# Optimization experiments

Measured on AMD Instinct MI355X. Metric: run time of the kernel, lower is better.

## Reference

```python
import jax, jax.numpy as jnp
import numpy as np

B, N, K = 8, 2048, 16          # clouds, points per cloud, knn k
C_IN, C_OUT, H = 64, 128, 64   # channels; H = hidden of pos_nn/attn_nn MLPs


def _init(key, shape, fan_in):
    return jax.random.normal(key, shape, jnp.float32) / np.sqrt(fan_in)


def setup_inputs() -> dict:
    key = jax.random.key(0)
    ks = jax.random.split(key, 20)
    P = B * N
    inp = {
        "x": jax.random.normal(ks[0], (P, C_IN), jnp.float32),
        "pos": jax.random.uniform(ks[1], (P, 3), jnp.float32),
        "batch": jnp.arange(P, dtype=jnp.int64 if jax.config.jax_enable_x64 else jnp.int32) // N,
        # lin_in: in->in, bias
        "Wi": _init(ks[2], (C_IN, C_IN), C_IN), "bi": jnp.zeros((C_IN,), jnp.float32),
        # PointTransformerConv: lin_src/lin_dst/lin are bias-free Linear(in, out)
        "Wsrc": _init(ks[3], (C_IN, C_OUT), C_IN),
        "Wdst": _init(ks[4], (C_IN, C_OUT), C_IN),
        "Wlin": _init(ks[5], (C_IN, C_OUT), C_IN),
        # pos_nn = MLP([3, 64, out], norm=None, plain_last=False): Lin-ReLU-Lin-ReLU
        "Wp1": _init(ks[6], (3, H), 3), "bp1": jnp.zeros((H,), jnp.float32),
        "Wp2": _init(ks[7], (H, C_OUT), H), "bp2": jnp.zeros((C_OUT,), jnp.float32),
        # attn_nn = MLP([out, 64, out], norm=None, plain_last=False)
        "Wa1": _init(ks[8], (C_OUT, H), C_OUT), "ba1": jnp.zeros((H,), jnp.float32),
        "Wa2": _init(ks[9], (H, C_OUT), H), "ba2": jnp.zeros((C_OUT,), jnp.float32),
        # lin_out: out->out, bias
        "Wo": _init(ks[10], (C_OUT, C_OUT), C_OUT), "bo": jnp.zeros((C_OUT,), jnp.float32),
    }
    return inp


def _knn_with_self(pn):
    # pn: [B,N,3] -> neighbor indices [B,N,K+1] = {self} U kNN (excl self),
    # matching knn_graph(loop=False) followed by conv's add_self_loops.
    sq = jnp.sum(pn * pn, -1)                                   # [B,N]
    d2 = sq[:, :, None] + sq[:, None, :] - 2.0 * jnp.einsum("bnd,bmd->bnm", pn, pn)
    d2 = d2 + jnp.eye(N, dtype=pn.dtype) * 1e10                 # exclude self
    _, idx = jax.lax.top_k(-d2, K)                              # [B,N,K]
    self_idx = jnp.broadcast_to(jnp.arange(N)[None, :, None], (B, N, 1))
    return jnp.concatenate([self_idx, idx], axis=-1)            # [B,N,K+1]


def _forward(x, pos, batch, Wi, bi, Wsrc, Wdst, Wlin, Wp1, bp1, Wp2, bp2,
             Wa1, ba1, Wa2, ba2, Wo, bo):
    # batch is structured as B equal-size clouds of N points (see setup_inputs);
    # knn is computed per-cloud, equivalent to knn_graph(pos, k, batch).
    h = jax.nn.relu(x @ Wi + bi).reshape(B, N, C_IN)            # lin_in + relu
    pn = pos.reshape(B, N, 3)
    nbr = _knn_with_self(pn)                                    # [B,N,K+1]

    gather = jax.vmap(lambda t, i: t[i])                        # [N,C],[N,K+1]->[N,K+1,C]

    a_src = h @ Wsrc                                            # [B,N,C_OUT]
    a_dst = h @ Wdst
    v = h @ Wlin

    rel = pn[:, :, None, :] - gather(pn, nbr)                   # pos_i - pos_j [B,N,K+1,3]
    delta = jax.nn.relu(jax.nn.relu(rel @ Wp1 + bp1) @ Wp2 + bp2)   # pos_nn

    alpha = a_dst[:, :, None, :] - gather(a_src, nbr) + delta   # alpha_i - alpha_j + delta
    attn = jax.nn.relu(jax.nn.relu(alpha @ Wa1 + ba1) @ Wa2 + ba2)  # attn_nn
    w = jax.nn.softmax(attn, axis=2)                            # softmax over neighbors

    msg = w * (gather(v, nbr) + delta)                          # [B,N,K+1,C_OUT]
    out = jnp.mean(msg, axis=2)                                 # aggr='mean' (PyG default here)
    out = out.reshape(B * N, C_OUT)
    return jax.nn.relu(out @ Wo + bo)                           # lin_out + relu


def reference(x, pos, batch, Wi, bi, Wsrc, Wdst, Wlin, Wp1, bp1, Wp2, bp2,
              Wa1, ba1, Wa2, ba2, Wo, bo):
    return _forward(x, pos, batch, Wi, bi, Wsrc, Wdst, Wlin, Wp1, bp1, Wp2, bp2,
                    Wa1, ba1, Wa2, ba2, Wo, bo)
```

## Files before the change

kernel.cpp:

```cpp
#include <hip/hip_runtime.h>
#include <hip/hip_fp16.h>

typedef _Float16 h8 __attribute__((ext_vector_type(8)));
typedef _Float16 h4 __attribute__((ext_vector_type(4)));
typedef float fx4 __attribute__((ext_vector_type(4)));

#define NPTS   2048
#define KP1    17
#define PGPT   4
#define EDGES  68
#define ROWS   80
#define MT     5
#define DELTA_OFF 0
#define PH_OFF    20480
#define ATT_OFF   30720
#define SJ_OFF    30720
#define NBR_OFF   52224
#define EDGE_SMEM 52544
#define ATT_RB    168

__device__ __forceinline__ int swzA(int row, int bytecol) {
  return (row << 7) + (bytecol ^ ((row & 7) << 4));
}
__device__ __forceinline__ int swzB(int row, int bytecol) {
  return (row << 8) + (bytecol ^ ((row & 7) << 4));
}

#define GH_NB    256
#define WP_NB    32
#define P1_GRID  (GH_NB + WP_NB)

__global__ __launch_bounds__(512) void phase1_kernel(
    const float* __restrict__ x, const float* __restrict__ Wi, const float* __restrict__ bi,
    float* __restrict__ h,
    const float* __restrict__ Wdst, const float* __restrict__ Wsrc,
    const float* __restrict__ Wlin, const float* __restrict__ Wa1,
    float* __restrict__ Wall)
{
  __shared__ __align__(16) char buf[33792];
  const int bid = blockIdx.x;
  const int tid = threadIdx.x;

  if (bid < GH_NB) {
    float* As = (float*)buf;
    float* Ws = (float*)(buf + 64 * 68 * 4);
    long row0 = (long)bid * 64;
    {
      int r = tid >> 3, k8 = (tid & 7) * 8;
      float4 a0 = *(const float4*)(x + (row0 + r) * 64 + k8);
      float4 a1 = *(const float4*)(x + (row0 + r) * 64 + k8 + 4);
      *(float4*)&As[r * 68 + k8] = a0;
      *(float4*)&As[r * 68 + k8 + 4] = a1;
      float4 w0 = *(const float4*)(Wi + r * 64 + k8);
      float4 w1 = *(const float4*)(Wi + r * 64 + k8 + 4);
      *(float4*)&Ws[r * 64 + k8] = w0;
      *(float4*)&Ws[r * 64 + k8 + 4] = w1;
    }
    __syncthreads();
    int tx = tid & 15, ty = tid >> 4;
    float acc[2][4] = {};
#pragma unroll 8
    for (int k = 0; k < 64; ++k) {
      float4 w = *(const float4*)&Ws[k * 64 + tx * 4];
      float a0 = As[(ty * 2 + 0) * 68 + k];
      float a1 = As[(ty * 2 + 1) * 68 + k];
      acc[0][0] += a0 * w.x; acc[0][1] += a0 * w.y; acc[0][2] += a0 * w.z; acc[0][3] += a0 * w.w;
      acc[1][0] += a1 * w.x; acc[1][1] += a1 * w.y; acc[1][2] += a1 * w.z; acc[1][3] += a1 * w.w;
    }
    float b0 = bi[tx * 4 + 0], b1 = bi[tx * 4 + 1], b2 = bi[tx * 4 + 2], b3 = bi[tx * 4 + 3];
#pragma unroll
    for (int i = 0; i < 2; ++i) {
      float4 o;
      o.x = fmaxf(acc[i][0] + b0, 0.f); o.y = fmaxf(acc[i][1] + b1, 0.f);
      o.z = fmaxf(acc[i][2] + b2, 0.f); o.w = fmaxf(acc[i][3] + b3, 0.f);
      *(float4*)(h + (row0 + ty * 2 + i) * 64 + tx * 4) = o;
    }
  } else {
    int gid = (bid - GH_NB) * 512 + tid;
    int q = gid >> 12, r = (gid >> 6) & 63, c = gid & 63;
    float val;
    if (q < 2) {
      const float* W = q ? Wsrc : Wdst;
      float acc = 0.f;
      for (int k = 0; k < 128; ++k) acc += W[r * 128 + k] * Wa1[k * 64 + c];
      val = acc;
    } else {
      val = Wlin[r * 128 + (q - 2) * 64 + c];
    }
    Wall[r * 256 + q * 64 + c] = val;
  }
}

#define KNN_NB 2048
#define UG_NB  1024
#define PK_NB  80
#define K2_GRID (KNN_NB + UG_NB + PK_NB)

__global__ __launch_bounds__(512) void knn_usv_kernel(
    const float* __restrict__ pos, int* __restrict__ nbr, float* __restrict__ rel,
    const float* __restrict__ h, const float* __restrict__ Wall,
    float* __restrict__ usv,
    const float* __restrict__ Wp2, const float* __restrict__ Wa1,
    const float* __restrict__ Wa2, const float* __restrict__ Wo,
    _Float16* __restrict__ p2p, _Float16* __restrict__ a1p, _Float16* __restrict__ a2p,
    _Float16* __restrict__ wop)
{
  __shared__ __align__(16) char buf[33792];
  const int bid = blockIdx.x;
  const int tid = threadIdx.x;

  if (bid < KNN_NB) {
    float* px  = (float*)buf;
    float* py  = (float*)(buf + 8192);
    float* pz  = (float*)(buf + 16384);
    float* sqs = (float*)(buf + 24576);
    int p0 = bid * 8;
    int base = (p0 >> 11) << 11;
    for (int i = tid; i < NPTS; i += 512) {
      float xx = pos[(size_t)(base + i) * 3 + 0];
      float yy = pos[(size_t)(base + i) * 3 + 1];
      float zz = pos[(size_t)(base + i) * 3 + 2];
      px[i] = xx; py[i] = yy; pz[i] = zz;
      sqs[i] = xx * xx + yy * yy + zz * zz;
    }
    __syncthreads();
    int wid = tid >> 6, lane = tid & 63;
    int pl = (p0 & 2047) + wid;
    int gp = base + pl;
    float pix = px[pl], piy = py[pl], piz = pz[pl];

    unsigned key[8];
#pragma unroll
    for (int i = 0; i < 8; ++i) key[i] = 0xFFFFFFFFu;
#pragma unroll
    for (int t = 0; t < 32; ++t) {
      int j = t * 64 + lane;
      float dot = pix * px[j] + piy * py[j] + piz * pz[j];
      float dp = __builtin_fmaf(-2.f, dot, sqs[j]) + 4.0f;
      unsigned kb = (__float_as_uint(dp) & 0xFFFFFFE0u) | (unsigned)t;
      kb = (j == pl) ? 0xFFFFFFFFu : kb;
#pragma unroll
      for (int i = 0; i < 8; ++i) {
        unsigned lo = min(key[i], kb), hi = max(key[i], kb);
        key[i] = lo; kb = hi;
      }
    }

    double pxd = (double)pix, pyd = (double)piy, pzd = (double)piz;
    double sqi64 = pxd * pxd + pyd * pyd + pzd * pzd;
    unsigned long long kk[8];
#pragma unroll
    for (int i = 0; i < 8; ++i) {
      if (key[i] == 0xFFFFFFFFu) { kk[i] = 0xFFFFFFFFFFFFFFFFull; continue; }
      int t = key[i] & 31;
      int j = t * 64 + lane;
      double xj = (double)px[j], yj = (double)py[j], zj = (double)pz[j];
      double sqj = xj * xj + yj * yj + zj * zj;
      double dot = pxd * xj + pyd * yj + pzd * zj;
      double d2 = sqi64 + sqj - 2.0 * dot;
      d2 = d2 > 0.0 ? d2 : 0.0;
      unsigned long long bits = (unsigned long long)__double_as_longlong(d2);
      kk[i] = (bits & ~0x7FFull) | (unsigned long long)j;
    }
#define CE(a, b) { unsigned long long lo_ = kk[a] < kk[b] ? kk[a] : kk[b]; \
                   unsigned long long hi_ = kk[a] < kk[b] ? kk[b] : kk[a]; \
                   kk[a] = lo_; kk[b] = hi_; }
    CE(0,1) CE(2,3) CE(4,5) CE(6,7)
    CE(0,2) CE(1,3) CE(4,6) CE(5,7)
    CE(1,2) CE(5,6) CE(0,4) CE(3,7)
    CE(1,5) CE(2,6)
    CE(1,4) CE(3,6)
    CE(2,4) CE(3,5)
    CE(3,4)
#undef CE

    if (lane == 0) nbr[gp * KP1] = gp;
    if (lane < 3)  rel[(size_t)gp * KP1 * 3 + lane] = 0.f;
    for (int it = 0; it < 16; ++it) {
      unsigned h32 = (unsigned)(kk[0] >> 32);
      unsigned key2 = (h32 & ~63u) | (unsigned)lane;
      unsigned m2 = key2;
#pragma unroll
      for (int off = 32; off > 0; off >>= 1) {
        unsigned o = __shfl_xor(m2, off);
        m2 = o < m2 ? o : m2;
      }
      bool same = ((key2 ^ m2) >> 6) == 0;
      unsigned long long ball = __ballot(same);
      int wl; unsigned jwin;
      if (__popcll(ball) == 1) {
        wl = (int)(m2 & 63u);
        unsigned lo32 = (unsigned)kk[0];
        unsigned wlo = __shfl(lo32, wl);
        jwin = wlo & 2047u;
      } else {
        unsigned long long mk = same ? kk[0] : 0xFFFFFFFFFFFFFFFFull;
#pragma unroll
        for (int off = 32; off > 0; off >>= 1) {
          unsigned long long o = __shfl_xor(mk, off);
          mk = o < mk ? o : mk;
        }
        jwin = (unsigned)(mk & 2047ull);
        wl = (int)(jwin & 63u);
      }
      if (lane == 0) nbr[gp * KP1 + 1 + it] = base + (int)jwin;
      if (lane < 3) {
        const float* ps = lane == 0 ? px : (lane == 1 ? py : pz);
        float pi = lane == 0 ? pix : (lane == 1 ? piy : piz);
        rel[((size_t)gp * KP1 + 1 + it) * 3 + lane] = pi - ps[(int)jwin];
      }
      bool mine = (lane == wl);
#pragma unroll
      for (int i = 0; i < 7; ++i) kk[i] = mine ? kk[i + 1] : kk[i];
      kk[7] = mine ? 0xFFFFFFFFFFFFFFFFull : kk[7];
    }
  } else if (bid < KNN_NB + UG_NB) {
    float* As = (float*)buf;
    float* Ws = (float*)(buf + 64 * 68 * 4);
    int b2 = bid - KNN_NB;
    long row0 = (long)(b2 >> 2) * 64;
    int c0 = (b2 & 3) * 64;
    {
      int r = tid >> 3, k8 = (tid & 7) * 8;
      float4 a0 = *(const float4*)(h + (row0 + r) * 64 + k8);
      float4 a1 = *(const float4*)(h + (row0 + r) * 64 + k8 + 4);
      *(float4*)&As[r * 68 + k8] = a0;
      *(float4*)&As[r * 68 + k8 + 4] = a1;
      float4 w0 = *(const float4*)(Wall + r * 256 + c0 + k8);
      float4 w1 = *(const float4*)(Wall + r * 256 + c0 + k8 + 4);
      *(float4*)&Ws[r * 64 + k8] = w0;
      *(float4*)&Ws[r * 64 + k8 + 4] = w1;
    }
    __syncthreads();
    int tx = tid & 15, ty = tid >> 4;
    float acc[2][4] = {};
#pragma unroll 8
    for (int k = 0; k < 64; ++k) {
      float4 w = *(const float4*)&Ws[k * 64 + tx * 4];
      float a0 = As[(ty * 2 + 0) * 68 + k];
      float a1 = As[(ty * 2 + 1) * 68 + k];
      acc[0][0] += a0 * w.x; acc[0][1] += a0 * w.y; acc[0][2] += a0 * w.z; acc[0][3] += a0 * w.w;
      acc[1][0] += a1 * w.x; acc[1][1] += a1 * w.y; acc[1][2] += a1 * w.z; acc[1][3] += a1 * w.w;
    }
#pragma unroll
    for (int i = 0; i < 2; ++i) {
      float4 o;
      o.x = acc[i][0]; o.y = acc[i][1]; o.z = acc[i][2]; o.w = acc[i][3];
      *(float4*)(usv + (row0 + ty * 2 + i) * 256 + c0 + tx * 4) = o;
    }
  } else {
    int gid = (bid - KNN_NB - UG_NB) * 512 + tid;
    if (gid < 24576) {
      int m = gid >> 13;
      int r = gid & 8191;
      int tl = r >> 9;
      int l  = (r >> 3) & 63;
      int j  = r & 7;
      const float* src; _Float16* dst; int N, kt, nt;
      if (m == 0)      { src = Wp2; dst = p2p; N = 128; kt = tl & 1; nt = tl >> 1; }
      else if (m == 1) { src = Wa1; dst = a1p; N = 64;  kt = tl & 3; nt = tl >> 2; }
      else             { src = Wa2; dst = a2p; N = 128; kt = tl & 1; nt = tl >> 1; }
      int k = kt * 32 + (l >> 4) * 8 + j;
      int n = nt * 16 + (l & 15);
      dst[r] = (_Float16)src[k * N + n];
    } else {
      int r = gid - 24576;
      int tl = r >> 9;
      int l  = (r >> 3) & 63;
      int j  = r & 7;
      int kt = tl & 3, nt = tl >> 2;
      int k = kt * 32 + (l >> 4) * 8 + j;
      int n = nt * 16 + (l & 15);
      wop[r] = (_Float16)Wo[k * 128 + n];
    }
  }
}

__global__ __launch_bounds__(512, 6) void edge_kernel(
    const int* __restrict__ nbr,
    const float* __restrict__ usv,
    const float* __restrict__ rel,
    const float* __restrict__ Wp1, const float* __restrict__ bp1,
    const float* __restrict__ bp2, const float* __restrict__ ba1, const float* __restrict__ ba2,
    const _Float16* __restrict__ Wp2p, const _Float16* __restrict__ Wa1p, const _Float16* __restrict__ Wa2p,
    const _Float16* __restrict__ Wop, const float* __restrict__ bo,
    float* __restrict__ out)
{
  __shared__ __align__(16) char smem[EDGE_SMEM];
  int* nbr_s = (int*)(smem + NBR_OFF);
  const int tid = threadIdx.x;
  const int lane = tid & 63;
  const int wid = tid >> 6;
  const int bid = blockIdx.x;
  const int pb = ((bid & 7) << 9) | (bid >> 3);
  const int p0 = pb * PGPT;

  const int pp5 = tid >> 7;
  const int c5 = tid & 127;
  float vreg[KP1];
  {
    const int* __restrict__ nrow = nbr + (size_t)(p0 + pp5) * KP1;
#pragma unroll
    for (int k = 0; k < KP1; ++k) {
      int jv = nrow[k];
      vreg[k] = usv[(size_t)jv * 256 + 128 + c5];
    }
  }

  if (tid < ROWS) nbr_s[tid] = (tid < EDGES) ? nbr[p0 * KP1 + tid] : p0;
  __syncthreads();

  {
    float w1x = Wp1[lane], w1y = Wp1[64 + lane], w1z = Wp1[128 + lane], b1 = bp1[lane];
    float b1a = ba1[lane];
    const float* relb = rel + (size_t)p0 * (KP1 * 3);
    for (int e = wid; e < ROWS; e += 8) {
      int eb = __builtin_amdgcn_readfirstlane(min(e, EDGES - 1));
      int p  = (eb * 241) >> 12;
      int j  = __builtin_amdgcn_readfirstlane(nbr_s[eb]);
      float sv = usv[(size_t)j * 256 + 64 + lane];
      float uu = usv[(size_t)(p0 + p) * 256 + lane];
      *(_Float16*)(smem + SJ_OFF + swzA(e, lane * 2)) = (_Float16)(uu - sv + b1a);
      float rx = relb[eb * 3 + 0];
      float ry = relb[eb * 3 + 1];
      float rz = relb[eb * 3 + 2];
      float acc = fmaxf(b1 + rx * w1x + ry * w1y + rz * w1z, 0.f);
      *(_Float16*)(smem + PH_OFF + swzA(e, lane * 2)) = (_Float16)acc;
    }
  }
  __syncthreads();

  const int rl = lane & 15;
  const int kl = lane >> 4;

  {
    int nt = wid;
    h8 b0 = *(const h8*)(Wp2p + ((size_t)(nt * 2 + 0) * 64 + lane) * 8);
    h8 b1 = *(const h8*)(Wp2p + ((size_t)(nt * 2 + 1) * 64 + lane) * 8);
    int col = nt * 16 + rl;
    float bias2 = bp2[col];
    for (int mt = 0; mt < MT; ++mt) {
      int arow = mt * 16 + rl;
      h8 a0 = *(const h8*)(smem + PH_OFF + swzA(arow, kl * 16));
      h8 a1 = *(const h8*)(smem + PH_OFF + swzA(arow, 64 + kl * 16));
      fx4 acc = {0.f, 0.f, 0.f, 0.f};
      acc = __builtin_amdgcn_mfma_f32_16x16x32_f16(a0, b0, acc, 0, 0, 0);
      acc = __builtin_amdgcn_mfma_f32_16x16x32_f16(a1, b1, acc, 0, 0, 0);
#pragma unroll
      for (int jj = 0; jj < 4; ++jj) {
        int orow = mt * 16 + kl * 4 + jj;
        float val = fmaxf(acc[jj] + bias2, 0.f);
        *(_Float16*)(smem + DELTA_OFF + swzB(orow, col * 2)) = (_Float16)val;
      }
    }
  }
  __syncthreads();

  {
    int nt = wid & 3;
    h8 b[4];
#pragma unroll
    for (int kt = 0; kt < 4; ++kt)
      b[kt] = *(const h8*)(Wa1p + ((size_t)(nt * 4 + kt) * 64 + lane) * 8);
    int hcol = nt * 16 + rl;
    for (int mt = (wid >> 2); mt < MT; mt += 2) {
      int arow = mt * 16 + rl;
      fx4 acc = {0.f, 0.f, 0.f, 0.f};
#pragma unroll
      for (int kt = 0; kt < 4; ++kt) {
        h8 a = *(const h8*)(smem + DELTA_OFF + swzB(arow, kt * 64 + kl * 16));
        acc = __builtin_amdgcn_mfma_f32_16x16x32_f16(a, b[kt], acc, 0, 0, 0);
      }
#pragma unroll
      for (int jj = 0; jj < 4; ++jj) {
        int orow = mt * 16 + kl * 4 + jj;
        float bb = (float)*(const _Float16*)(smem + SJ_OFF + swzA(orow, hcol * 2));
        float val = fmaxf(acc[jj] + bb, 0.f);
        *(_Float16*)(smem + PH_OFF + swzA(orow, hcol * 2)) = (_Float16)val;
      }
    }
  }
  __syncthreads();

  {
    int nt = wid;
    h8 b0 = *(const h8*)(Wa2p + ((size_t)(nt * 2 + 0) * 64 + lane) * 8);
    h8 b1 = *(const h8*)(Wa2p + ((size_t)(nt * 2 + 1) * 64 + lane) * 8);
    int col = nt * 16 + rl;
    float b2v = ba2[col];
    char* cbase = smem + ATT_OFF + col * ATT_RB;
    for (int mt = 0; mt < MT; ++mt) {
      int arow = mt * 16 + rl;
      h8 a0 = *(const h8*)(smem + PH_OFF + swzA(arow, kl * 16));
      h8 a1 = *(const h8*)(smem + PH_OFF + swzA(arow, 64 + kl * 16));
      fx4 acc = {0.f, 0.f, 0.f, 0.f};
      acc = __builtin_amdgcn_mfma_f32_16x16x32_f16(a0, b0, acc, 0, 0, 0);
      acc = __builtin_amdgcn_mfma_f32_16x16x32_f16(a1, b1, acc, 0, 0, 0);
#pragma unroll
      for (int jj = 0; jj < 4; ++jj) {
        int orow = mt * 16 + kl * 4 + jj;
        if (orow < EDGES) {
          int pp = (orow * 241) >> 12;
          float val = fmaxf(acc[jj] + b2v, 0.f);
          *(_Float16*)(cbase + (orow + 3 * pp) * 2) = (_Float16)val;
        }
      }
    }
  }
  __syncthreads();

  h8 bw[4];
#pragma unroll
  for (int kt = 0; kt < 4; ++kt)
    bw[kt] = *(const h8*)(Wop + ((size_t)(wid * 4 + kt) * 64 + lane) * 8);

  {
    int r0 = pp5 * KP1;
    const char* abase = smem + ATT_OFF + c5 * ATT_RB + pp5 * 40;
    h4 t0 = *(const h4*)(abase + 0);
    h4 t1 = *(const h4*)(abase + 8);
    h4 t2 = *(const h4*)(abase + 16);
    h4 t3 = *(const h4*)(abase + 24);
    float att[KP1];
#pragma unroll
    for (int q = 0; q < 4; ++q) {
      att[0 + q]  = (float)t0[q];
      att[4 + q]  = (float)t1[q];
      att[8 + q]  = (float)t2[q];
      att[12 + q] = (float)t3[q];
    }
    att[16] = (float)*(const _Float16*)(abase + 32);
    float m8[8];
#pragma unroll
    for (int k = 0; k < 8; ++k) m8[k] = fmaxf(att[k], att[k + 8]);
    float m4a = fmaxf(m8[0], m8[1]), m4b = fmaxf(m8[2], m8[3]);
    float m4c = fmaxf(m8[4], m8[5]), m4d = fmaxf(m8[6], m8[7]);
    float m = fmaxf(fmaxf(fmaxf(m4a, m4b), fmaxf(m4c, m4d)), att[16]);
    float den = 0.f;
#pragma unroll
    for (int k = 0; k < KP1; ++k) { att[k] = __expf(att[k] - m); den += att[k]; }
    float inv = 1.f / (den * 17.f);
    float acc = 0.f;
#pragma unroll
    for (int k = 0; k < KP1; ++k) {
      float dd = (float)*(const _Float16*)(smem + DELTA_OFF + swzB(r0 + k, c5 * 2));
      acc += att[k] * (vreg[k] + dd);
    }
    *(_Float16*)(smem + PH_OFF + swzB(pp5, c5 * 2)) = (_Float16)(acc * inv);
  }
  __syncthreads();

  {
    fx4 acc = {0.f, 0.f, 0.f, 0.f};
#pragma unroll
    for (int kt = 0; kt < 4; ++kt) {
      h8 a = *(const h8*)(smem + PH_OFF + swzB(rl, kt * 64 + kl * 16));
      acc = __builtin_amdgcn_mfma_f32_16x16x32_f16(a, bw[kt], acc, 0, 0, 0);
    }
    if (kl == 0) {
      int col = wid * 16 + rl;
      float bov = bo[col];
#pragma unroll
      for (int jj = 0; jj < 4; ++jj)
        out[(size_t)(p0 + jj) * 128 + col] = fmaxf(acc[jj] + bov, 0.f);
    }
  }
}

extern "C" void kernel_launch(void* const* d_in, const int* in_sizes, int n_in,
                              void* d_out, int out_size, void* d_ws, size_t ws_size,
                              hipStream_t stream) {
  const float* x    = (const float*)d_in[0];
  const float* pos  = (const float*)d_in[1];
  const float* Wi   = (const float*)d_in[3];
  const float* bi   = (const float*)d_in[4];
  const float* Wsrc = (const float*)d_in[5];
  const float* Wdst = (const float*)d_in[6];
  const float* Wlin = (const float*)d_in[7];
  const float* Wp1  = (const float*)d_in[8];
  const float* bp1  = (const float*)d_in[9];
  const float* Wp2  = (const float*)d_in[10];
  const float* bp2  = (const float*)d_in[11];
  const float* Wa1  = (const float*)d_in[12];
  const float* ba1  = (const float*)d_in[13];
  const float* Wa2  = (const float*)d_in[14];
  const float* ba2  = (const float*)d_in[15];
  const float* Wo   = (const float*)d_in[16];
  const float* bo   = (const float*)d_in[17];
  float* out = (float*)d_out;

  char* ws = (char*)d_ws;
  float* h    = (float*)(ws + 0);
  float* usv  = (float*)(ws + 4194304);
  float* Wall = (float*)(ws + 20971520);
  float* rel  = (float*)(ws + 21037056);
  int*   nbr  = (int*)  (ws + 29360128);
  _Float16* p2p = (_Float16*)(ws + 30474240);
  _Float16* a1p = (_Float16*)(ws + 30490624);
  _Float16* a2p = (_Float16*)(ws + 30507008);
  _Float16* wop = (_Float16*)(ws + 30523392);

  phase1_kernel<<<P1_GRID, 512, 0, stream>>>(x, Wi, bi, h, Wdst, Wsrc, Wlin, Wa1, Wall);
  knn_usv_kernel<<<K2_GRID, 512, 0, stream>>>(pos, nbr, rel, h, Wall, usv,
                                              Wp2, Wa1, Wa2, Wo, p2p, a1p, a2p, wop);
  edge_kernel<<<4096, 512, 0, stream>>>(nbr, usv, rel, Wp1, bp1, bp2, ba1, ba2,
                                        p2p, a1p, a2p, wop, bo, out);
}
```

Measured before the change: 136.9 us.

## Co-schedule kNN with h and weight prep, split usv GEMM into own kernel

```diff
diff --git a/kernel.cpp b/kernel.cpp
--- a/kernel.cpp
+++ b/kernel.cpp
@@ -26,82 +26,21 @@
   return (row << 8) + (bytecol ^ ((row & 7) << 4));
 }
 
-#define GH_NB    256
-#define WP_NB    32
-#define P1_GRID  (GH_NB + WP_NB)
-
-__global__ __launch_bounds__(512) void phase1_kernel(
+#define KNN_NB 2048
+#define GH_NB  256
+#define WP_NB  32
+#define PK_NB  80
+#define A_GRID (KNN_NB + GH_NB + WP_NB + PK_NB)
+
+__global__ __launch_bounds__(512) void frontA_kernel(
+    const float* __restrict__ pos, int* __restrict__ nbr, float* __restrict__ rel,
     const float* __restrict__ x, const float* __restrict__ Wi, const float* __restrict__ bi,
     float* __restrict__ h,
     const float* __restrict__ Wdst, const float* __restrict__ Wsrc,
     const float* __restrict__ Wlin, const float* __restrict__ Wa1,
-    float* __restrict__ Wall)
-{
-  __shared__ __align__(16) char buf[33792];
-  const int bid = blockIdx.x;
-  const int tid = threadIdx.x;
-
-  if (bid < GH_NB) {
-    float* As = (float*)buf;
-    float* Ws = (float*)(buf + 64 * 68 * 4);
-    long row0 = (long)bid * 64;
-    {
-      int r = tid >> 3, k8 = (tid & 7) * 8;
-      float4 a0 = *(const float4*)(x + (row0 + r) * 64 + k8);
-      float4 a1 = *(const float4*)(x + (row0 + r) * 64 + k8 + 4);
-      *(float4*)&As[r * 68 + k8] = a0;
-      *(float4*)&As[r * 68 + k8 + 4] = a1;
-      float4 w0 = *(const float4*)(Wi + r * 64 + k8);
-      float4 w1 = *(const float4*)(Wi + r * 64 + k8 + 4);
-      *(float4*)&Ws[r * 64 + k8] = w0;
-      *(float4*)&Ws[r * 64 + k8 + 4] = w1;
-    }
-    __syncthreads();
-    int tx = tid & 15, ty = tid >> 4;
-    float acc[2][4] = {};
-#pragma unroll 8
-    for (int k = 0; k < 64; ++k) {
-      float4 w = *(const float4*)&Ws[k * 64 + tx * 4];
-      float a0 = As[(ty * 2 + 0) * 68 + k];
-      float a1 = As[(ty * 2 + 1) * 68 + k];
-      acc[0][0] += a0 * w.x; acc[0][1] += a0 * w.y; acc[0][2] += a0 * w.z; acc[0][3] += a0 * w.w;
-      acc[1][0] += a1 * w.x; acc[1][1] += a1 * w.y; acc[1][2] += a1 * w.z; acc[1][3] += a1 * w.w;
-    }
-    float b0 = bi[tx * 4 + 0], b1 = bi[tx * 4 + 1], b2 = bi[tx * 4 + 2], b3 = bi[tx * 4 + 3];
-#pragma unroll
-    for (int i = 0; i < 2; ++i) {
-      float4 o;
-      o.x = fmaxf(acc[i][0] + b0, 0.f); o.y = fmaxf(acc[i][1] + b1, 0.f);
-      o.z = fmaxf(acc[i][2] + b2, 0.f); o.w = fmaxf(acc[i][3] + b3, 0.f);
-      *(float4*)(h + (row0 + ty * 2 + i) * 64 + tx * 4) = o;
-    }
-  } else {
-    int gid = (bid - GH_NB) * 512 + tid;
-    int q = gid >> 12, r = (gid >> 6) & 63, c = gid & 63;
-    float val;
-    if (q < 2) {
-      const float* W = q ? Wsrc : Wdst;
-      float acc = 0.f;
-      for (int k = 0; k < 128; ++k) acc += W[r * 128 + k] * Wa1[k * 64 + c];
-      val = acc;
-    } else {
-      val = Wlin[r * 128 + (q - 2) * 64 + c];
-    }
-    Wall[r * 256 + q * 64 + c] = val;
-  }
-}
-
-#define KNN_NB 2048
-#define UG_NB  1024
-#define PK_NB  80
-#define K2_GRID (KNN_NB + UG_NB + PK_NB)
-
-__global__ __launch_bounds__(512) void knn_usv_kernel(
-    const float* __restrict__ pos, int* __restrict__ nbr, float* __restrict__ rel,
-    const float* __restrict__ h, const float* __restrict__ Wall,
-    float* __restrict__ usv,
-    const float* __restrict__ Wp2, const float* __restrict__ Wa1,
-    const float* __restrict__ Wa2, const float* __restrict__ Wo,
+    float* __restrict__ Wall,
+    const float* __restrict__ Wp2, const float* __restrict__ Wa2,
+    const float* __restrict__ Wo,
     _Float16* __restrict__ p2p, _Float16* __restrict__ a1p, _Float16* __restrict__ a2p,
     _Float16* __restrict__ wop)
 {
@@ -110,24 +49,22 @@
   const int tid = threadIdx.x;
 
   if (bid < KNN_NB) {
-    float* px  = (float*)buf;
-    float* py  = (float*)(buf + 8192);
-    float* pz  = (float*)(buf + 16384);
-    float* sqs = (float*)(buf + 24576);
+    float4* pc = (float4*)buf;
     int p0 = bid * 8;
     int base = (p0 >> 11) << 11;
     for (int i = tid; i < NPTS; i += 512) {
       float xx = pos[(size_t)(base + i) * 3 + 0];
       float yy = pos[(size_t)(base + i) * 3 + 1];
       float zz = pos[(size_t)(base + i) * 3 + 2];
-      px[i] = xx; py[i] = yy; pz[i] = zz;
-      sqs[i] = xx * xx + yy * yy + zz * zz;
+      float4 v; v.x = xx; v.y = yy; v.z = zz; v.w = xx * xx + yy * yy + zz * zz;
+      pc[i] = v;
     }
     __syncthreads();
     int wid = tid >> 6, lane = tid & 63;
     int pl = (p0 & 2047) + wid;
     int gp = base + pl;
-    float pix = px[pl], piy = py[pl], piz = pz[pl];
+    float4 qp = pc[pl];
+    float pix = qp.x, piy = qp.y, piz = qp.z;
 
     unsigned key[8];
 #pragma unroll
@@ -135,8 +72,9 @@
 #pragma unroll
     for (int t = 0; t < 32; ++t) {
       int j = t * 64 + lane;
-      float dot = pix * px[j] + piy * py[j] + piz * pz[j];
-      float dp = __builtin_fmaf(-2.f, dot, sqs[j]) + 4.0f;
+      float4 c = pc[j];
+      float dot = pix * c.x + piy * c.y + piz * c.z;
+      float dp = __builtin_fmaf(-2.f, dot, c.w) + 4.0f;
       unsigned kb = (__float_as_uint(dp) & 0xFFFFFFE0u) | (unsigned)t;
       kb = (j == pl) ? 0xFFFFFFFFu : kb;
 #pragma unroll
@@ -154,7 +92,8 @@
       if (key[i] == 0xFFFFFFFFu) { kk[i] = 0xFFFFFFFFFFFFFFFFull; continue; }
       int t = key[i] & 31;
       int j = t * 64 + lane;
-      double xj = (double)px[j], yj = (double)py[j], zj = (double)pz[j];
+      float4 c = pc[j];
+      double xj = (double)c.x, yj = (double)c.y, zj = (double)c.z;
       double sqj = xj * xj + yj * yj + zj * zj;
       double dot = pxd * xj + pyd * yj + pzd * zj;
       double d2 = sqi64 + sqj - 2.0 * dot;
@@ -205,29 +144,27 @@
       }
       if (lane == 0) nbr[gp * KP1 + 1 + it] = base + (int)jwin;
       if (lane < 3) {
-        const float* ps = lane == 0 ? px : (lane == 1 ? py : pz);
         float pi = lane == 0 ? pix : (lane == 1 ? piy : piz);
-        rel[((size_t)gp * KP1 + 1 + it) * 3 + lane] = pi - ps[(int)jwin];
+        float pj = ((const float*)&pc[(int)jwin])[lane];
+        rel[((size_t)gp * KP1 + 1 + it) * 3 + lane] = pi - pj;
       }
       bool mine = (lane == wl);
 #pragma unroll
       for (int i = 0; i < 7; ++i) kk[i] = mine ? kk[i + 1] : kk[i];
       kk[7] = mine ? 0xFFFFFFFFFFFFFFFFull : kk[7];
     }
-  } else if (bid < KNN_NB + UG_NB) {
+  } else if (bid < KNN_NB + GH_NB) {
     float* As = (float*)buf;
     float* Ws = (float*)(buf + 64 * 68 * 4);
-    int b2 = bid - KNN_NB;
-    long row0 = (long)(b2 >> 2) * 64;
-    int c0 = (b2 & 3) * 64;
+    long row0 = (long)(bid - KNN_NB) * 64;
     {
       int r = tid >> 3, k8 = (tid & 7) * 8;
-      float4 a0 = *(const float4*)(h + (row0 + r) * 64 + k8);
-      float4 a1 = *(const float4*)(h + (row0 + r) * 64 + k8 + 4);
+      float4 a0 = *(const float4*)(x + (row0 + r) * 64 + k8);
+      float4 a1 = *(const float4*)(x + (row0 + r) * 64 + k8 + 4);
       *(float4*)&As[r * 68 + k8] = a0;
       *(float4*)&As[r * 68 + k8 + 4] = a1;
-      float4 w0 = *(const float4*)(Wall + r * 256 + c0 + k8);
-      float4 w1 = *(const float4*)(Wall + r * 256 + c0 + k8 + 4);
+      float4 w0 = *(const float4*)(Wi + r * 64 + k8);
+      float4 w1 = *(const float4*)(Wi + r * 64 + k8 + 4);
       *(float4*)&Ws[r * 64 + k8] = w0;
       *(float4*)&Ws[r * 64 + k8 + 4] = w1;
     }
@@ -242,14 +179,29 @@
       acc[0][0] += a0 * w.x; acc[0][1] += a0 * w.y; acc[0][2] += a0 * w.z; acc[0][3] += a0 * w.w;
       acc[1][0] += a1 * w.x; acc[1][1] += a1 * w.y; acc[1][2] += a1 * w.z; acc[1][3] += a1 * w.w;
     }
+    float b0 = bi[tx * 4 + 0], b1 = bi[tx * 4 + 1], b2 = bi[tx * 4 + 2], b3 = bi[tx * 4 + 3];
 #pragma unroll
     for (int i = 0; i < 2; ++i) {
       float4 o;
-      o.x = acc[i][0]; o.y = acc[i][1]; o.z = acc[i][2]; o.w = acc[i][3];
-      *(float4*)(usv + (row0 + ty * 2 + i) * 256 + c0 + tx * 4) = o;
-    }
+      o.x = fmaxf(acc[i][0] + b0, 0.f); o.y = fmaxf(acc[i][1] + b1, 0.f);
+      o.z = fmaxf(acc[i][2] + b2, 0.f); o.w = fmaxf(acc[i][3] + b3, 0.f);
+      *(float4*)(h + (row0 + ty * 2 + i) * 64 + tx * 4) = o;
+    }
+  } else if (bid < KNN_NB + GH_NB + WP_NB) {
+    int gid = (bid - KNN_NB - GH_NB) * 512 + tid;
+    int q = gid >> 12, r = (gid >> 6) & 63, c = gid & 63;
+    float val;
+    if (q < 2) {
+      const float* W = q ? Wsrc : Wdst;
+      float acc = 0.f;
+      for (int k = 0; k < 128; ++k) acc += W[r * 128 + k] * Wa1[k * 64 + c];
+      val = acc;
+    } else {
+      val = Wlin[r * 128 + (q - 2) * 64 + c];
+    }
+    Wall[r * 256 + q * 64 + c] = val;
   } else {
-    int gid = (bid - KNN_NB - UG_NB) * 512 + tid;
+    int gid = (bid - KNN_NB - GH_NB - WP_NB) * 512 + tid;
     if (gid < 24576) {
       int m = gid >> 13;
       int r = gid & 8191;
@@ -276,6 +228,47 @@
   }
 }
 
+__global__ __launch_bounds__(512) void usv_kernel(
+    const float* __restrict__ h, const float* __restrict__ Wall,
+    float* __restrict__ usv)
+{
+  __shared__ __align__(16) char buf[33792];
+  const int tid = threadIdx.x;
+  float* As = (float*)buf;
+  float* Ws = (float*)(buf + 64 * 68 * 4);
+  int b2 = blockIdx.x;
+  long row0 = (long)(b2 >> 2) * 64;
+  int c0 = (b2 & 3) * 64;
+  {
+    int r = tid >> 3, k8 = (tid & 7) * 8;
+    float4 a0 = *(const float4*)(h + (row0 + r) * 64 + k8);
+    float4 a1 = *(const float4*)(h + (row0 + r) * 64 + k8 + 4);
+    *(float4*)&As[r * 68 + k8] = a0;
+    *(float4*)&As[r * 68 + k8 + 4] = a1;
+    float4 w0 = *(const float4*)(Wall + r * 256 + c0 + k8);
+    float4 w1 = *(const float4*)(Wall + r * 256 + c0 + k8 + 4);
+    *(float4*)&Ws[r * 64 + k8] = w0;
+    *(float4*)&Ws[r * 64 + k8 + 4] = w1;
+  }
+  __syncthreads();
+  int tx = tid & 15, ty = tid >> 4;
+  float acc[2][4] = {};
+#pragma unroll 8
+  for (int k = 0; k < 64; ++k) {
+    float4 w = *(const float4*)&Ws[k * 64 + tx * 4];
+    float a0 = As[(ty * 2 + 0) * 68 + k];
+    float a1 = As[(ty * 2 + 1) * 68 + k];
+    acc[0][0] += a0 * w.x; acc[0][1] += a0 * w.y; acc[0][2] += a0 * w.z; acc[0][3] += a0 * w.w;
+    acc[1][0] += a1 * w.x; acc[1][1] += a1 * w.y; acc[1][2] += a1 * w.z; acc[1][3] += a1 * w.w;
+  }
+#pragma unroll
+  for (int i = 0; i < 2; ++i) {
+    float4 o;
+    o.x = acc[i][0]; o.y = acc[i][1]; o.z = acc[i][2]; o.w = acc[i][3];
+    *(float4*)(usv + (row0 + ty * 2 + i) * 256 + c0 + tx * 4) = o;
+  }
+}
+
 __global__ __launch_bounds__(512, 6) void edge_kernel(
     const int* __restrict__ nbr,
     const float* __restrict__ usv,
@@ -500,9 +493,10 @@
   _Float16* a2p = (_Float16*)(ws + 30507008);
   _Float16* wop = (_Float16*)(ws + 30523392);
 
-  phase1_kernel<<<P1_GRID, 512, 0, stream>>>(x, Wi, bi, h, Wdst, Wsrc, Wlin, Wa1, Wall);
-  knn_usv_kernel<<<K2_GRID, 512, 0, stream>>>(pos, nbr, rel, h, Wall, usv,
-                                              Wp2, Wa1, Wa2, Wo, p2p, a1p, a2p, wop);
+  frontA_kernel<<<A_GRID, 512, 0, stream>>>(pos, nbr, rel, x, Wi, bi, h,
+                                            Wdst, Wsrc, Wlin, Wa1, Wall,
+                                            Wp2, Wa2, Wo, p2p, a1p, a2p, wop);
+  usv_kernel<<<1024, 512, 0, stream>>>(h, Wall, usv);
   edge_kernel<<<4096, 512, 0, stream>>>(nbr, usv, rel, Wp1, bp1, bp2, ba1, ba2,
                                         p2p, a1p, a2p, wop, bo, out);
 }
```

After: 149.0 us. +8.8%, slower.
